# Kernel optimization log

Hardware: AMD Instinct MI355X
Metric: run time of the kernel (lower is better)

Reference implementation:

```python
import jax, jax.numpy as jnp
from jax import lax
import numpy as np

N_ITER = 50  # entmax.EntmaxBisect default n_iter


def _p(z, alpha):
    # inverse of g'(t) = t**(alpha-1): clamp then fractional power
    return jnp.maximum(z, 0.0) ** (1.0 / (alpha - 1.0))


def entmax_bisect(x, alpha):
    """alpha-entmax over the last axis via 50-step bisection (entmax.EntmaxBisect)."""
    am1 = alpha - 1.0
    X = x * am1
    d = X.shape[-1]
    max_val = jnp.max(X, axis=-1, keepdims=True)
    tau_lo = max_val - 1.0                    # max - _gp(1, alpha)
    tau_hi = max_val - (1.0 / d) ** am1       # max - _gp(1/d, alpha)
    f_lo = jnp.sum(_p(X - tau_lo, alpha), axis=-1, keepdims=True) - 1.0
    dm0 = tau_hi - tau_lo

    def body(i, carry):
        dm, tlo, _ = carry
        dm = dm / 2.0
        tau_m = tlo + dm
        p_m = _p(X - tau_m, alpha)
        f_m = jnp.sum(p_m, axis=-1, keepdims=True) - 1.0
        mask = (f_m * f_lo) >= 0.0
        tlo = jnp.where(mask, tau_m, tlo)
        return dm, tlo, p_m

    _, _, p_m = lax.fori_loop(0, N_ITER, body, (dm0, tau_lo, jnp.zeros_like(X)))
    # ensure_sum_one=True
    return p_m / jnp.sum(p_m, axis=-1, keepdims=True)


def setup_inputs() -> dict:
    key = jax.random.key(0)
    in_value = jax.random.normal(key, (2048, 32000), dtype=jnp.float32)
    alpha = jnp.asarray(1.5, dtype=jnp.float32)  # the q parameter
    return {"in_value": in_value, "alpha": alpha}


def reference(in_value, alpha):
    return entmax_bisect(in_value, alpha)
```

## Files before the change

### kernel.cpp

```cpp
#include <hip/hip_runtime.h>
#include <math.h>


#define D_DIM   32000
#define NV4     (D_DIM / 4)
#define BLOCK   512
#define NWAVE   (BLOCK / 64)
#define NCHUNK  16
#define CAP     6144
#define NEWTON_MAX 30
#define NITER   50

typedef float f32x4 __attribute__((ext_vector_type(4)));

__device__ __forceinline__ float wave_sum(float v) {
#pragma unroll
    for (int off = 32; off > 0; off >>= 1) v += __shfl_xor(v, off, 64);
    return v;
}
__device__ __forceinline__ float wave_max(float v) {
#pragma unroll
    for (int off = 32; off > 0; off >>= 1) v = fmaxf(v, __shfl_xor(v, off, 64));
    return v;
}
__device__ __forceinline__ float pf(float z, bool sq, float expo) {
    z = fmaxf(z, 0.0f);
    return sq ? z * z : powf(z, expo);
}
__device__ __forceinline__ unsigned fflip(float f) {
    unsigned u = __float_as_uint(f);
    return u ^ ((u >> 31) ? 0xFFFFFFFFu : 0x80000000u);
}
__device__ __forceinline__ float funflip(unsigned u) {
    return __uint_as_float(u ^ ((u & 0x80000000u) ? 0x80000000u : 0xFFFFFFFFu));
}

__global__ __launch_bounds__(BLOCK, 2)
void entmax_bisect_kernel(const float* __restrict__ x,
                          const float* __restrict__ alpha_p,
                          float* __restrict__ out) {
    const int row  = blockIdx.x;
    const int tid  = threadIdx.x;
    const int lane = tid & 63;
    const int wid  = tid >> 6;

    __shared__ float    s_val[CAP];
    __shared__ float    s_red[NWAVE];
    __shared__ float    s_bc[2];
    __shared__ int      s_cnt;
    __shared__ unsigned s_gmax;

    const float alpha   = alpha_p[0];
    const float am1     = alpha - 1.0f;
    const float inv_am1 = 1.0f / am1;
    const float expo    = inv_am1;
    const bool  sq      = (expo == 2.0f);

    const float* __restrict__ rowp = x + (size_t)row * D_DIM;
    const float4* __restrict__ x4  = (const float4*)rowp;
    float4*       __restrict__ o4  = (float4*)(out + (size_t)row * D_DIM);

    if (tid == 0) { s_cnt = 0; s_gmax = 0u; }
    __syncthreads();

    f32x4 v[NCHUNK];
#pragma unroll
    for (int k = 0; k < NCHUNK; ++k) {
        const int i4   = tid + (k << 9);
        const int safe = (i4 < NV4) ? i4 : (NV4 - 1);
        const unsigned boff = (unsigned)safe * 16u;
        asm volatile("global_load_dwordx4 %0, %1, %2"
                     : "=v"(v[k]) : "v"(boff), "s"(rowp));
    }
    asm volatile("s_waitcnt vmcnt(0)" ::: "memory");
    __builtin_amdgcn_sched_barrier(0);
#pragma unroll
    for (int k = 0; k < NCHUNK; ++k)
        if (tid + (k << 9) >= NV4)
            v[k] = (f32x4){-INFINITY, -INFINITY, -INFINITY, -INFINITY};

    float tm = -INFINITY;
#pragma unroll
    for (int k = 0; k < NCHUNK; ++k)
        tm = fmaxf(tm, fmaxf(fmaxf(v[k][0], v[k][1]), fmaxf(v[k][2], v[k][3])));
    const float wm  = wave_max(tm);
    const float wmX = wm * am1;
    if (lane == 0) atomicMax(&s_gmax, fflip(wmX));
    const unsigned r = __hip_atomic_load(&s_gmax, __ATOMIC_RELAXED,
                                         __HIP_MEMORY_SCOPE_WORKGROUP);
    const float run   = fmaxf(funflip(r), wmX);
    const float thr_x = (run - 1.0f) * inv_am1;

    int cnt = 0;
#pragma unroll
    for (int k = 0; k < NCHUNK; ++k) {
        cnt += (v[k][0] > thr_x) + (v[k][1] > thr_x)
             + (v[k][2] > thr_x) + (v[k][3] > thr_x);
    }
    int inc = cnt;
#pragma unroll
    for (int off = 1; off < 64; off <<= 1) {
        const int t = __shfl_up(inc, off, 64);
        if (lane >= off) inc += t;
    }
    const int total = __shfl(inc, 63, 64);
    if (total > 0) {
        int base = 0;
        if (lane == 63) base = atomicAdd(&s_cnt, total);
        base = __shfl(base, 63, 64);
        int pos = base + (inc - cnt);
        auto append1 = [&](float val) {
            if (val > thr_x) {
                if (pos < CAP) s_val[pos] = val * am1;
                ++pos;
            }
        };
#pragma unroll
        for (int k = 0; k < NCHUNK; ++k) {
            append1(v[k][0]); append1(v[k][1]);
            append1(v[k][2]); append1(v[k][3]);
        }
    }
    __syncthreads();
    const int   n_act   = s_cnt;
    const float max_val = funflip(s_gmax);
    const float tau_lo0 = max_val - 1.0f;

    if (n_act <= CAP) {
        if (wid == 0) {
            float tau, S;
            if (sq) {
                tau = tau_lo0;
                for (int it = 0; it < NEWTON_MAX; ++it) {
                    float s1 = 0.f, s2 = 0.f;
                    for (int i = lane; i < n_act; i += 64) {
                        const float z = fmaxf(s_val[i] - tau, 0.f);
                        s1 += z; s2 += z * z;
                    }
#pragma unroll
                    for (int off = 32; off > 0; off >>= 1) {
                        s1 += __shfl_xor(s1, off, 64);
                        s2 += __shfl_xor(s2, off, 64);
                    }
                    const float dtau = (s2 - 1.0f) / fmaxf(2.0f * s1, 1e-30f);
                    tau += dtau;
                    if (dtau < 1e-7f * fmaxf(1.0f, fabsf(tau))) break;
                }
                float s2 = 0.f;
                for (int i = lane; i < n_act; i += 64) {
                    const float z = fmaxf(s_val[i] - tau, 0.f);
                    s2 += z * z;
                }
                S = wave_sum(s2);
            } else {
                const float tau_hi = max_val - powf(1.0f / (float)D_DIM, am1);
                float dm = tau_hi - tau_lo0;
                float s = 0.f;
                for (int i = lane; i < n_act; i += 64)
                    s += pf(s_val[i] - tau_lo0, sq, expo);
                s = wave_sum(s);
                const float f_lo = s - 1.0f;
                float tlo = tau_lo0, tau_m = tau_lo0, fsum = s;
                for (int it = 0; it < NITER; ++it) {
                    dm *= 0.5f;
                    tau_m = tlo + dm;
                    float t = 0.f;
                    for (int i = lane; i < n_act; i += 64)
                        t += pf(s_val[i] - tau_m, sq, expo);
                    t = wave_sum(t);
                    fsum = t;
                    if ((t - 1.0f) * f_lo >= 0.0f) tlo = tau_m;
                }
                tau = tau_m; S = fsum;
            }
            if (lane == 0) { s_bc[0] = tau; s_bc[1] = S; }
        }
        __syncthreads();

        const float tau_f = s_bc[0];
        const float invS  = 1.0f / s_bc[1];
#pragma unroll
        for (int k = 0; k < NCHUNK; ++k) {
            const int i4 = tid + (k << 9);
            if (i4 < NV4) {
                float4 o;
                {
                    const float z = fmaxf(v[k][0] * am1 - tau_f, 0.f);
                    o.x = (sq ? z * z : powf(z, expo)) * invS;
                }
                {
                    const float z = fmaxf(v[k][1] * am1 - tau_f, 0.f);
                    o.y = (sq ? z * z : powf(z, expo)) * invS;
                }
                {
                    const float z = fmaxf(v[k][2] * am1 - tau_f, 0.f);
                    o.z = (sq ? z * z : powf(z, expo)) * invS;
                }
                {
                    const float z = fmaxf(v[k][3] * am1 - tau_f, 0.f);
                    o.w = (sq ? z * z : powf(z, expo)) * invS;
                }
                o4[i4] = o;
            }
        }
    } else {
        const float tau_hi = max_val - powf(1.0f / (float)D_DIM, am1);
        float dm = tau_hi - tau_lo0;
        float s = 0.f;
        for (int i4 = tid; i4 < NV4; i4 += BLOCK) {
            float4 vv = x4[i4];
            s += pf(vv.x * am1 - tau_lo0, sq, expo) + pf(vv.y * am1 - tau_lo0, sq, expo)
               + pf(vv.z * am1 - tau_lo0, sq, expo) + pf(vv.w * am1 - tau_lo0, sq, expo);
        }
        s = wave_sum(s);
        __syncthreads();
        if (lane == 0) s_red[wid] = s;
        __syncthreads();
        float tot = 0.f;
#pragma unroll
        for (int w = 0; w < NWAVE; ++w) tot += s_red[w];
        const float f_lo = tot - 1.0f;
        float tlo = tau_lo0, tau_m = tau_lo0, fsum = tot;
        for (int it = 0; it < NITER; ++it) {
            dm *= 0.5f;
            tau_m = tlo + dm;
            float t = 0.f;
            for (int i4 = tid; i4 < NV4; i4 += BLOCK) {
                float4 vv = x4[i4];
                t += pf(vv.x * am1 - tau_m, sq, expo) + pf(vv.y * am1 - tau_m, sq, expo)
                   + pf(vv.z * am1 - tau_m, sq, expo) + pf(vv.w * am1 - tau_m, sq, expo);
            }
            t = wave_sum(t);
            __syncthreads();
            if (lane == 0) s_red[wid] = t;
            __syncthreads();
            float tt = 0.f;
#pragma unroll
            for (int w = 0; w < NWAVE; ++w) tt += s_red[w];
            fsum = tt;
            if ((tt - 1.0f) * f_lo >= 0.0f) tlo = tau_m;
        }
        const float invS = 1.0f / fsum;
        for (int i4 = tid; i4 < NV4; i4 += BLOCK) {
            float4 vv = x4[i4];
            float4 o;
            o.x = pf(vv.x * am1 - tau_m, sq, expo) * invS;
            o.y = pf(vv.y * am1 - tau_m, sq, expo) * invS;
            o.z = pf(vv.z * am1 - tau_m, sq, expo) * invS;
            o.w = pf(vv.w * am1 - tau_m, sq, expo) * invS;
            o4[i4] = o;
        }
    }
}

extern "C" void kernel_launch(void* const* d_in, const int* in_sizes, int n_in,
                              void* d_out, int out_size, void* d_ws, size_t ws_size,
                              hipStream_t stream) {
    const float* x       = (const float*)d_in[0];
    const float* alpha_p = (const float*)d_in[1];
    float* out           = (float*)d_out;
    const int rows       = in_sizes[0] / D_DIM;
    entmax_bisect_kernel<<<rows, BLOCK, 0, stream>>>(x, alpha_p, out);
}
```

Measured before the change: 449.2 us.

## Process four rows per block with double-buffered register prefetch of next row

Each block now handles four rows and, while computing one row, issues the global loads for the next row into a second register buffer, overlapping HBM latency with the threshold solve. The data layout changes to a contiguous per-wave slice. When few elements are active, the solve keeps them in registers instead of re-reading LDS, and the fallback path reuses register-held data instead of re-reading global memory. Double buffering doubles register pressure (two 64-float arrays) and reduces the grid to 512 blocks, which may hurt occupancy or spill.

```diff
diff --git a/kernel.cpp b/kernel.cpp
--- a/kernel.cpp
+++ b/kernel.cpp
@@ -2,14 +2,17 @@
 #include <math.h>
 
 
-#define D_DIM   32000
-#define NV4     (D_DIM / 4)
-#define BLOCK   512
-#define NWAVE   (BLOCK / 64)
-#define NCHUNK  16
-#define CAP     6144
+#define D_DIM    32000
+#define NV4      8000
+#define BLOCK    512
+#define NWAVE    8
+#define NCHUNK   16
+#define PER_WAVE 1000
+#define RPB      4
+#define CAP      6144
+#define NCREG    8
 #define NEWTON_MAX 30
-#define NITER   50
+#define NITER    50
 
 typedef float f32x4 __attribute__((ext_vector_type(4)));
 
@@ -35,98 +38,161 @@
     return __uint_as_float(u ^ ((u & 0x80000000u) ? 0x80000000u : 0xFFFFFFFFu));
 }
 
-__global__ __launch_bounds__(BLOCK, 2)
-void entmax_bisect_kernel(const float* __restrict__ x,
-                          const float* __restrict__ alpha_p,
-                          float* __restrict__ out) {
-    const int row  = blockIdx.x;
-    const int tid  = threadIdx.x;
-    const int lane = tid & 63;
-    const int wid  = tid >> 6;
-
-    __shared__ float    s_val[CAP];
-    __shared__ float    s_red[NWAVE];
-    __shared__ float    s_bc[2];
-    __shared__ int      s_cnt;
-    __shared__ unsigned s_gmax;
-
-    const float alpha   = alpha_p[0];
-    const float am1     = alpha - 1.0f;
-    const float inv_am1 = 1.0f / am1;
-    const float expo    = inv_am1;
-    const bool  sq      = (expo == 2.0f);
-
-    const float* __restrict__ rowp = x + (size_t)row * D_DIM;
-    const float4* __restrict__ x4  = (const float4*)rowp;
-    float4*       __restrict__ o4  = (float4*)(out + (size_t)row * D_DIM);
-
-    if (tid == 0) { s_cnt = 0; s_gmax = 0u; }
-    __syncthreads();
-
-    f32x4 v[NCHUNK];
-#pragma unroll
-    for (int k = 0; k < NCHUNK; ++k) {
-        const int i4   = tid + (k << 9);
-        const int safe = (i4 < NV4) ? i4 : (NV4 - 1);
-        const unsigned boff = (unsigned)safe * 16u;
-        asm volatile("global_load_dwordx4 %0, %1, %2"
-                     : "=v"(v[k]) : "v"(boff), "s"(rowp));
-    }
+__device__ __forceinline__ void block_sync_lds() {
+    asm volatile("s_waitcnt lgkmcnt(0)" ::: "memory");
+    __builtin_amdgcn_s_barrier();
+    asm volatile("" ::: "memory");
+}
+__device__ __forceinline__ void wait_vm0() {
     asm volatile("s_waitcnt vmcnt(0)" ::: "memory");
     __builtin_amdgcn_sched_barrier(0);
+}
+
+__device__ __forceinline__ void issue_loads(f32x4 (&dst)[NCHUNK],
+                                            const float* __restrict__ rowp,
+                                            int lane, int wid) {
+#pragma unroll
+    for (int k = 0; k < NCHUNK; ++k) {
+        const int off = (k << 6) + lane;
+        const int i4  = wid * PER_WAVE + ((off < PER_WAVE) ? off : PER_WAVE - 1);
+        const unsigned boff = (unsigned)i4 * 16u;
+        asm volatile("global_load_dwordx4 %0, %1, %2"
+                     : "=v"(dst[k]) : "v"(boff), "s"(rowp) : "memory");
+    }
+}
+
+struct SMem {
+    float    val[CAP];
+    float    red[NWAVE];
+    float    bc[2];
+    int      cnt[2];
+    unsigned gmax[2];
+};
+
+template<bool ISSUE_NEXT>
+__device__ __forceinline__ void row_step(
+    const float* __restrict__ x, float* __restrict__ out,
+    int row, int next_ldrow, int n_rows, int p,
+    f32x4 (&cur)[NCHUNK], f32x4 (&nxt)[NCHUNK],
+    int tid, int lane, int wid,
+    float am1, float inv_am1, float expo, bool sq, SMem& sm)
+{
+    wait_vm0();
+    if constexpr (ISSUE_NEXT)
+        issue_loads(nxt, x + (size_t)next_ldrow * D_DIM, lane, wid);
+    if (row >= n_rows) return;
+
 #pragma unroll
     for (int k = 0; k < NCHUNK; ++k)
-        if (tid + (k << 9) >= NV4)
-            v[k] = (f32x4){-INFINITY, -INFINITY, -INFINITY, -INFINITY};
+        if ((k << 6) + lane >= PER_WAVE)
+            cur[k] = (f32x4){-INFINITY, -INFINITY, -INFINITY, -INFINITY};
 
     float tm = -INFINITY;
 #pragma unroll
     for (int k = 0; k < NCHUNK; ++k)
-        tm = fmaxf(tm, fmaxf(fmaxf(v[k][0], v[k][1]), fmaxf(v[k][2], v[k][3])));
+        tm = fmaxf(tm, fmaxf(fmaxf(cur[k][0], cur[k][1]),
+                             fmaxf(cur[k][2], cur[k][3])));
     const float wm  = wave_max(tm);
     const float wmX = wm * am1;
-    if (lane == 0) atomicMax(&s_gmax, fflip(wmX));
-    const unsigned r = __hip_atomic_load(&s_gmax, __ATOMIC_RELAXED,
-                                         __HIP_MEMORY_SCOPE_WORKGROUP);
-    const float run   = fmaxf(funflip(r), wmX);
+    if (lane == 0) atomicMax(&sm.gmax[p], fflip(wmX));
+    const unsigned rr = __hip_atomic_load(&sm.gmax[p], __ATOMIC_RELAXED,
+                                          __HIP_MEMORY_SCOPE_WORKGROUP);
+    const float run   = fmaxf(funflip(rr), wmX);
     const float thr_x = (run - 1.0f) * inv_am1;
 
     int cnt = 0;
 #pragma unroll
-    for (int k = 0; k < NCHUNK; ++k) {
-        cnt += (v[k][0] > thr_x) + (v[k][1] > thr_x)
-             + (v[k][2] > thr_x) + (v[k][3] > thr_x);
-    }
+    for (int k = 0; k < NCHUNK; ++k)
+        cnt += (cur[k][0] > thr_x) + (cur[k][1] > thr_x)
+             + (cur[k][2] > thr_x) + (cur[k][3] > thr_x);
     int inc = cnt;
 #pragma unroll
     for (int off = 1; off < 64; off <<= 1) {
         const int t = __shfl_up(inc, off, 64);
         if (lane >= off) inc += t;
     }
-    const int total = __shfl(inc, 63, 64);
-    if (total > 0) {
+    const int wtotal = __shfl(inc, 63, 64);
+    if (wtotal > 0) {
         int base = 0;
-        if (lane == 63) base = atomicAdd(&s_cnt, total);
+        if (lane == 63) base = atomicAdd(&sm.cnt[p], wtotal);
         base = __shfl(base, 63, 64);
         int pos = base + (inc - cnt);
-        auto append1 = [&](float val) {
-            if (val > thr_x) {
-                if (pos < CAP) s_val[pos] = val * am1;
-                ++pos;
+#pragma unroll
+        for (int k = 0; k < NCHUNK; ++k)
+#pragma unroll
+            for (int c = 0; c < 4; ++c) {
+                const float val = cur[k][c];
+                if (val > thr_x) {
+                    if (pos < CAP) sm.val[pos] = val * am1;
+                    ++pos;
+                }
             }
-        };
-#pragma unroll
-        for (int k = 0; k < NCHUNK; ++k) {
-            append1(v[k][0]); append1(v[k][1]);
-            append1(v[k][2]); append1(v[k][3]);
+    }
+    block_sync_lds();
+
+    const int   n_act   = sm.cnt[p];
+    const float max_val = funflip(sm.gmax[p]);
+    if (tid == 0) { sm.cnt[p ^ 1] = 0; sm.gmax[p ^ 1] = 0u; }
+    const float tau_lo0 = max_val - 1.0f;
+
+    if (n_act <= NCREG * 64) {
+        if (wid == 0) {
+            float c[NCREG];
+#pragma unroll
+            for (int j = 0; j < NCREG; ++j) {
+                const int idx = (j << 6) + lane;
+                c[j] = (idx < n_act) ? sm.val[idx] : -INFINITY;
+            }
+            float tau, S;
+            if (sq) {
+                tau = tau_lo0;
+                for (int it = 0; it < NEWTON_MAX; ++it) {
+                    float s1 = 0.f, s2 = 0.f;
+#pragma unroll
+                    for (int j = 0; j < NCREG; ++j) {
+                        const float z = fmaxf(c[j] - tau, 0.f);
+                        s1 += z; s2 += z * z;
+                    }
+#pragma unroll
+                    for (int off = 32; off > 0; off >>= 1) {
+                        s1 += __shfl_xor(s1, off, 64);
+                        s2 += __shfl_xor(s2, off, 64);
+                    }
+                    const float dtau = (s2 - 1.0f) / fmaxf(2.0f * s1, 1e-30f);
+                    tau += dtau;
+                    if (dtau < 1e-7f * fmaxf(1.0f, fabsf(tau))) break;
+                }
+                float s2 = 0.f;
+#pragma unroll
+                for (int j = 0; j < NCREG; ++j) {
+                    const float z = fmaxf(c[j] - tau, 0.f);
+                    s2 += z * z;
+                }
+                S = wave_sum(s2);
+            } else {
+                const float tau_hi = max_val - powf(1.0f / (float)D_DIM, am1);
+                float dm = tau_hi - tau_lo0;
+                float s = 0.f;
+#pragma unroll
+                for (int j = 0; j < NCREG; ++j) s += pf(c[j] - tau_lo0, sq, expo);
+                s = wave_sum(s);
+                const float f_lo = s - 1.0f;
+                float tlo = tau_lo0, tau_m = tau_lo0, fsum = s;
+                for (int it = 0; it < NITER; ++it) {
+                    dm *= 0.5f;
+                    tau_m = tlo + dm;
+                    float t = 0.f;
+#pragma unroll
+                    for (int j = 0; j < NCREG; ++j) t += pf(c[j] - tau_m, sq, expo);
+                    t = wave_sum(t);
+                    fsum = t;
+                    if ((t - 1.0f) * f_lo >= 0.0f) tlo = tau_m;
+                }
+                tau = tau_m; S = fsum;
+            }
+            if (lane == 0) { sm.bc[0] = tau; sm.bc[1] = S; }
         }
-    }
-    __syncthreads();
-    const int   n_act   = s_cnt;
-    const float max_val = funflip(s_gmax);
-    const float tau_lo0 = max_val - 1.0f;
-
-    if (n_act <= CAP) {
+    } else if (n_act <= CAP) {
         if (wid == 0) {
             float tau, S;
             if (sq) {
@@ -134,7 +200,7 @@
                 for (int it = 0; it < NEWTON_MAX; ++it) {
                     float s1 = 0.f, s2 = 0.f;
                     for (int i = lane; i < n_act; i += 64) {
-                        const float z = fmaxf(s_val[i] - tau, 0.f);
+                        const float z = fmaxf(sm.val[i] - tau, 0.f);
                         s1 += z; s2 += z * z;
                     }
 #pragma unroll
@@ -148,7 +214,7 @@
                 }
                 float s2 = 0.f;
                 for (int i = lane; i < n_act; i += 64) {
-                    const float z = fmaxf(s_val[i] - tau, 0.f);
+                    const float z = fmaxf(sm.val[i] - tau, 0.f);
                     s2 += z * z;
                 }
                 S = wave_sum(s2);
@@ -157,7 +223,7 @@
                 float dm = tau_hi - tau_lo0;
                 float s = 0.f;
                 for (int i = lane; i < n_act; i += 64)
-                    s += pf(s_val[i] - tau_lo0, sq, expo);
+                    s += pf(sm.val[i] - tau_lo0, sq, expo);
                 s = wave_sum(s);
                 const float f_lo = s - 1.0f;
                 float tlo = tau_lo0, tau_m = tau_lo0, fsum = s;
@@ -166,91 +232,109 @@
                     tau_m = tlo + dm;
                     float t = 0.f;
                     for (int i = lane; i < n_act; i += 64)
-                        t += pf(s_val[i] - tau_m, sq, expo);
+                        t += pf(sm.val[i] - tau_m, sq, expo);
                     t = wave_sum(t);
                     fsum = t;
                     if ((t - 1.0f) * f_lo >= 0.0f) tlo = tau_m;
                 }
                 tau = tau_m; S = fsum;
             }
-            if (lane == 0) { s_bc[0] = tau; s_bc[1] = S; }
-        }
-        __syncthreads();
-
-        const float tau_f = s_bc[0];
-        const float invS  = 1.0f / s_bc[1];
-#pragma unroll
-        for (int k = 0; k < NCHUNK; ++k) {
-            const int i4 = tid + (k << 9);
-            if (i4 < NV4) {
-                float4 o;
-                {
-                    const float z = fmaxf(v[k][0] * am1 - tau_f, 0.f);
-                    o.x = (sq ? z * z : powf(z, expo)) * invS;
-                }
-                {
-                    const float z = fmaxf(v[k][1] * am1 - tau_f, 0.f);
-                    o.y = (sq ? z * z : powf(z, expo)) * invS;
-                }
-                {
-                    const float z = fmaxf(v[k][2] * am1 - tau_f, 0.f);
-                    o.z = (sq ? z * z : powf(z, expo)) * invS;
-                }
-                {
-                    const float z = fmaxf(v[k][3] * am1 - tau_f, 0.f);
-                    o.w = (sq ? z * z : powf(z, expo)) * invS;
-                }
-                o4[i4] = o;
-            }
+            if (lane == 0) { sm.bc[0] = tau; sm.bc[1] = S; }
         }
     } else {
         const float tau_hi = max_val - powf(1.0f / (float)D_DIM, am1);
         float dm = tau_hi - tau_lo0;
-        float s = 0.f;
-        for (int i4 = tid; i4 < NV4; i4 += BLOCK) {
-            float4 vv = x4[i4];
-            s += pf(vv.x * am1 - tau_lo0, sq, expo) + pf(vv.y * am1 - tau_lo0, sq, expo)
-               + pf(vv.z * am1 - tau_lo0, sq, expo) + pf(vv.w * am1 - tau_lo0, sq, expo);
-        }
-        s = wave_sum(s);
-        __syncthreads();
-        if (lane == 0) s_red[wid] = s;
-        __syncthreads();
+        float sacc = 0.f;
+#pragma unroll
+        for (int k = 0; k < NCHUNK; ++k)
+#pragma unroll
+            for (int c = 0; c < 4; ++c)
+                sacc += pf(cur[k][c] * am1 - tau_lo0, sq, expo);
+        sacc = wave_sum(sacc);
+        if (lane == 0) sm.red[wid] = sacc;
+        block_sync_lds();
         float tot = 0.f;
 #pragma unroll
-        for (int w = 0; w < NWAVE; ++w) tot += s_red[w];
+        for (int w = 0; w < NWAVE; ++w) tot += sm.red[w];
         const float f_lo = tot - 1.0f;
         float tlo = tau_lo0, tau_m = tau_lo0, fsum = tot;
         for (int it = 0; it < NITER; ++it) {
+            block_sync_lds();
             dm *= 0.5f;
             tau_m = tlo + dm;
             float t = 0.f;
-            for (int i4 = tid; i4 < NV4; i4 += BLOCK) {
-                float4 vv = x4[i4];
-                t += pf(vv.x * am1 - tau_m, sq, expo) + pf(vv.y * am1 - tau_m, sq, expo)
-                   + pf(vv.z * am1 - tau_m, sq, expo) + pf(vv.w * am1 - tau_m, sq, expo);
-            }
+#pragma unroll
+            for (int k = 0; k < NCHUNK; ++k)
+#pragma unroll
+                for (int c = 0; c < 4; ++c)
+                    t += pf(cur[k][c] * am1 - tau_m, sq, expo);
             t = wave_sum(t);
-            __syncthreads();
-            if (lane == 0) s_red[wid] = t;
-            __syncthreads();
+            if (lane == 0) sm.red[wid] = t;
+            block_sync_lds();
             float tt = 0.f;
 #pragma unroll
-            for (int w = 0; w < NWAVE; ++w) tt += s_red[w];
+            for (int w = 0; w < NWAVE; ++w) tt += sm.red[w];
             fsum = tt;
             if ((tt - 1.0f) * f_lo >= 0.0f) tlo = tau_m;
         }
-        const float invS = 1.0f / fsum;
-        for (int i4 = tid; i4 < NV4; i4 += BLOCK) {
-            float4 vv = x4[i4];
+        if (tid == 0) { sm.bc[0] = tau_m; sm.bc[1] = fsum; }
+    }
+    block_sync_lds();
+
+    const float tau_f = sm.bc[0];
+    const float invS  = 1.0f / sm.bc[1];
+    float4* __restrict__ o4 = (float4*)(out + (size_t)row * D_DIM);
+#pragma unroll
+    for (int k = 0; k < NCHUNK; ++k) {
+        const int off = (k << 6) + lane;
+        if (off < PER_WAVE) {
+            const int i4 = wid * PER_WAVE + off;
             float4 o;
-            o.x = pf(vv.x * am1 - tau_m, sq, expo) * invS;
-            o.y = pf(vv.y * am1 - tau_m, sq, expo) * invS;
-            o.z = pf(vv.z * am1 - tau_m, sq, expo) * invS;
-            o.w = pf(vv.w * am1 - tau_m, sq, expo) * invS;
+            { const float z = fmaxf(cur[k][0] * am1 - tau_f, 0.f);
+              o.x = (sq ? z * z : powf(z, expo)) * invS; }
+            { const float z = fmaxf(cur[k][1] * am1 - tau_f, 0.f);
+              o.y = (sq ? z * z : powf(z, expo)) * invS; }
+            { const float z = fmaxf(cur[k][2] * am1 - tau_f, 0.f);
+              o.z = (sq ? z * z : powf(z, expo)) * invS; }
+            { const float z = fmaxf(cur[k][3] * am1 - tau_f, 0.f);
+              o.w = (sq ? z * z : powf(z, expo)) * invS; }
             o4[i4] = o;
         }
     }
+}
+
+__global__ __launch_bounds__(BLOCK, 2)
+void entmax_bisect_kernel(const float* __restrict__ x,
+                          const float* __restrict__ alpha_p,
+                          float* __restrict__ out, int n_rows) {
+    __shared__ SMem sm;
+    const int tid  = threadIdx.x;
+    const int lane = tid & 63;
+    const int wid  = tid >> 6;
+    const int row0 = blockIdx.x * RPB;
+
+    f32x4 vA[NCHUNK], vB[NCHUNK];
+
+    const int ld0 = (row0 < n_rows) ? row0 : (n_rows - 1);
+    issue_loads(vA, x + (size_t)ld0 * D_DIM, lane, wid);
+
+    const float alpha   = alpha_p[0];
+    const float am1     = alpha - 1.0f;
+    const float inv_am1 = 1.0f / am1;
+    const float expo    = inv_am1;
+    const bool  sq      = (expo == 2.0f);
+
+    if (tid == 0) { sm.cnt[0] = 0; sm.cnt[1] = 0; sm.gmax[0] = 0u; sm.gmax[1] = 0u; }
+    block_sync_lds();
+
+    const int r1 = (row0 + 1 < n_rows) ? row0 + 1 : n_rows - 1;
+    const int r2 = (row0 + 2 < n_rows) ? row0 + 2 : n_rows - 1;
+    const int r3 = (row0 + 3 < n_rows) ? row0 + 3 : n_rows - 1;
+
+    row_step<true >(x, out, row0,     r1, n_rows, 0, vA, vB, tid, lane, wid, am1, inv_am1, expo, sq, sm);
+    row_step<true >(x, out, row0 + 1, r2, n_rows, 1, vB, vA, tid, lane, wid, am1, inv_am1, expo, sq, sm);
+    row_step<true >(x, out, row0 + 2, r3, n_rows, 0, vA, vB, tid, lane, wid, am1, inv_am1, expo, sq, sm);
+    row_step<false>(x, out, row0 + 3, r3, n_rows, 1, vB, vA, tid, lane, wid, am1, inv_am1, expo, sq, sm);
 }
 
 extern "C" void kernel_launch(void* const* d_in, const int* in_sizes, int n_in,
@@ -260,5 +344,6 @@
     const float* alpha_p = (const float*)d_in[1];
     float* out           = (float*)d_out;
     const int rows       = in_sizes[0] / D_DIM;
-    entmax_bisect_kernel<<<rows, BLOCK, 0, stream>>>(x, alpha_p, out);
-}
+    const int nblocks    = (rows + RPB - 1) / RPB;
+    entmax_bisect_kernel<<<nblocks, BLOCK, 0, stream>>>(x, alpha_p, out, rows);
+}
```

Result: slower. 587.7 us (+30.8%).
